# Kernel optimization log

Measured on AMD Instinct MI355X. Metric: run time of the kernel, lower is better.

The kernel has to match this reference:

```python
import jax, jax.numpy as jnp
import numpy as np

D_MODEL = 768
N_HEADS = 12
D_K = D_MODEL // N_HEADS
NEG = -1e9


def setup_inputs() -> dict:
    key = jax.random.key(0)
    ks = jax.random.split(key, 9)
    B, S = 4, 2048
    s = 1.0 / np.sqrt(D_MODEL)
    inp = {
        "x": jax.random.normal(ks[0], (B, S, D_MODEL), dtype=jnp.float32),
        "mask": jnp.tril(jnp.ones((S, S), dtype=jnp.int32))[None, None, :, :],
        "Wq": jax.random.normal(ks[1], (D_MODEL, D_MODEL), dtype=jnp.float32) * s,
        "bq": jnp.zeros((D_MODEL,), dtype=jnp.float32),
        "Wk": jax.random.normal(ks[2], (D_MODEL, D_MODEL), dtype=jnp.float32) * s,
        "bk": jnp.zeros((D_MODEL,), dtype=jnp.float32),
        "Wv": jax.random.normal(ks[3], (D_MODEL, D_MODEL), dtype=jnp.float32) * s,
        "bv": jnp.zeros((D_MODEL,), dtype=jnp.float32),
        "Wo": jax.random.normal(ks[4], (D_MODEL, D_MODEL), dtype=jnp.float32) * s,
        "bo": jnp.zeros((D_MODEL,), dtype=jnp.float32),
    }
    return inp


def reference(x, mask, Wq, bq, Wk, bk, Wv, bv, Wo, bo):
    B, S, _ = x.shape
    # projections; weights stored [in, out] so y = x @ W + b
    def proj(W, b):
        return (x @ W + b).reshape(B, S, N_HEADS, D_K).transpose(0, 2, 1, 3)  # [B,H,S,Dk]
    q = proj(Wq, bq)
    k = proj(Wk, bk)
    v = proj(Wv, bv)
    scores = jnp.einsum("bhsd,bhtd->bhst", q, k) / jnp.sqrt(jnp.float32(D_K))
    scores = jnp.where(mask == 0, jnp.float32(NEG), scores)
    probs = jax.nn.softmax(scores, axis=-1)  # dropout is identity in eval mode
    ctx = jnp.einsum("bhst,bhtd->bhsd", probs, v)
    ctx = ctx.transpose(0, 2, 1, 3).reshape(B, S, D_MODEL)
    return ctx @ Wo + bo
```

## Files before the change

### kernel.cpp

```cpp
#include <hip/hip_runtime.h>
#include <hip/hip_bf16.h>

#define D_MODEL 768
#define NH 12
#define DK 64
#define SL 2048
#define BB 4
#define QL2E 0.18033688011112042f

typedef __attribute__((ext_vector_type(8))) short bf16x8;
typedef __attribute__((ext_vector_type(4))) float f32x4;

__device__ __forceinline__ unsigned short f2bf(float f) {
    unsigned u = __float_as_uint(f);
    u += 0x7FFFu + ((u >> 16) & 1u);
    return (unsigned short)(u >> 16);
}
__device__ __forceinline__ unsigned pkbf(float a, float b) {
    __hip_bfloat162 h = __float22bfloat162_rn(make_float2(a, b));
    unsigned u; __builtin_memcpy(&u, &h, 4); return u;
}
__device__ __forceinline__ void gll16(const unsigned short* g, unsigned short* l) {
    __builtin_amdgcn_global_load_lds(
        (const __attribute__((address_space(1))) unsigned int*)g,
        (__attribute__((address_space(3))) unsigned int*)l, 16, 0, 0);
}

__global__ __launch_bounds__(256)
void prep_kernel(const float* __restrict__ x, unsigned short* __restrict__ xb,
                 const float* __restrict__ Wq, const float* __restrict__ Wk,
                 const float* __restrict__ Wv, const float* __restrict__ Wo,
                 unsigned short* __restrict__ Wqkv_t,
                 unsigned short* __restrict__ Wo_t)
{
    __shared__ float t[32][33];
    const int bid = blockIdx.x;
    const int tid = threadIdx.x;
    if (bid < 6144) {
        const size_t i = ((size_t)bid * 256 + tid) * 4;
        float4 v = *(const float4*)(x + i);
        *(uint2*)(xb + i) = make_uint2(pkbf(v.x, v.y), pkbf(v.z, v.w));
    } else {
        const int nb = bid - 6144;
        const int z  = nb / 576;
        const int rem = nb - z * 576;
        const int k0 = (rem / 24) * 32, n0 = (rem % 24) * 32;
        const float* W = (z == 0) ? Wq : (z == 1) ? Wk : (z == 2) ? Wv : Wo;
        unsigned short* Wt = (z < 3) ? (Wqkv_t + (size_t)z * 768 * 768) : Wo_t;
        const int tx = tid & 31, ty = tid >> 5;
        #pragma unroll
        for (int i = 0; i < 4; ++i)
            t[ty + 8 * i][tx] = W[(size_t)(k0 + ty + 8 * i) * 768 + n0 + tx];
        __syncthreads();
        #pragma unroll
        for (int i = 0; i < 4; ++i)
            Wt[(size_t)(n0 + ty + 8 * i) * 768 + k0 + tx] = f2bf(t[tx][ty + 8 * i]);
    }
}

#define GEMM_DECLS                                                             \
    const int tid  = threadIdx.x;                                              \
    const int wv   = tid >> 6;                                                 \
    const int lane = tid & 63;                                                 \
    const int l15  = lane & 15;                                                \
    const int quad = lane >> 4;                                                \
    const int wm = wv >> 1, wn = wv & 1;                                       \
    (void)wm; (void)wn;

#define GEMM_LOOP(Ap, Bp)                                                      \
    f32x4 acc[4][4];                                                           \
    _Pragma("unroll")                                                          \
    for (int i = 0; i < 4; ++i)                                                \
        _Pragma("unroll")                                                      \
        for (int j = 0; j < 4; ++j) acc[i][j] = (f32x4){0.f, 0.f, 0.f, 0.f};   \
    auto stageg = [&](int k0, int bi) {                                        \
        _Pragma("unroll")                                                      \
        for (int t = 0; t < 2; ++t) {                                          \
            const int cib = wv * 128 + t * 64;                                 \
            const int ci  = cib + lane;                                        \
            gll16(Ap + (size_t)(bm + (ci >> 2)) * 768 + k0 + (ci & 3) * 8,     \
                  &smem[bi][cib * 8]);                                         \
            gll16(Bp + (size_t)(bn + (ci >> 2)) * 768 + k0 + (ci & 3) * 8,     \
                  &smem[2 + bi][cib * 8]);                                     \
        }                                                                      \
    };                                                                         \
    stageg(0, 0);                                                              \
    for (int k0 = 0; k0 < 768; k0 += 32) {                                     \
        __syncthreads();                                                       \
        if (k0 + 32 < 768) stageg(k0 + 32, ((k0 >> 5) + 1) & 1);               \
        const int bi = (k0 >> 5) & 1;                                          \
        bf16x8 af[4], bfr[4];                                                  \
        _Pragma("unroll")                                                      \
        for (int mt = 0; mt < 4; ++mt)                                         \
            af[mt] = *(const bf16x8*)&smem[bi][(wm * 64 + mt * 16 + l15) * 32 + quad * 8]; \
        _Pragma("unroll")                                                      \
        for (int nt = 0; nt < 4; ++nt)                                         \
            bfr[nt] = *(const bf16x8*)&smem[2 + bi][(wn * 64 + nt * 16 + l15) * 32 + quad * 8]; \
        _Pragma("unroll")                                                      \
        for (int mt = 0; mt < 4; ++mt)                                         \
            _Pragma("unroll")                                                  \
            for (int nt = 0; nt < 4; ++nt)                                     \
                acc[mt][nt] = __builtin_amdgcn_mfma_f32_16x16x32_bf16(         \
                    af[mt], bfr[nt], acc[mt][nt], 0, 0, 0);                    \
    }

__global__ __launch_bounds__(256)
void gemm_qkv(const unsigned short* __restrict__ Wt,
              const unsigned short* __restrict__ X,
              const unsigned short* __restrict__ Wvt,
              const float* __restrict__ bq, const float* __restrict__ bk,
              const float* __restrict__ bv,
              unsigned short* __restrict__ Qo, unsigned short* __restrict__ Ko,
              unsigned short* __restrict__ Vo)
{
    __shared__ unsigned short smem[4][128 * 32];
    const int bid = blockIdx.x;
    GEMM_DECLS

    if (bid < 768) {
        const int bm = (bid / 64) * 128;
        const int bn = (bid % 64) * 128;
        GEMM_LOOP(Wt, X)

        const int proj = (bm >= 768);
        const float osc = proj ? 1.0f : QL2E;
        const float* bias = proj ? bk : bq;
        unsigned short* out = proj ? Ko : Qo;
        const int mb0 = bm - proj * 768;

        unsigned short* se = &smem[0][0];
        unsigned short* ew = se + wv * 4096;
        __syncthreads();
        #pragma unroll
        for (int nt = 0; nt < 4; ++nt) {
            const int row = nt * 16 + l15;
            #pragma unroll
            for (int mt = 0; mt < 4; ++mt) {
                const int ml = mb0 + wm * 64 + mt * 16 + quad * 4;
                const float4 bb = *(const float4*)&bias[ml];
                const float v0 = (acc[mt][nt][0] + bb.x) * osc;
                const float v1 = (acc[mt][nt][1] + bb.y) * osc;
                const float v2 = (acc[mt][nt][2] + bb.z) * osc;
                const float v3 = (acc[mt][nt][3] + bb.w) * osc;
                const int s   = mt * 4 + quad;
                const int ssw = s ^ ((l15 & 7) << 1);
                *(uint2*)(ew + row * 64 + ssw * 4) =
                    make_uint2(pkbf(v0, v1), pkbf(v2, v3));
            }
        }
        __syncthreads();
        const int h0 = mb0 >> 6;
        #pragma unroll
        for (int p = 0; p < 8; ++p) {
            const int g    = p * 256 + tid;
            const int c    = g & 7;
            const int s128 = (g >> 3) & 127;
            const int hh   = g >> 10;
            const int row  = s128 & 63;
            const bf16x8 val = *(const bf16x8*)(se + (hh * 2 + (s128 >> 6)) * 4096 +
                                row * 64 + ((c ^ (row & 7)) * 8));
            const int sg = bn + s128;
            const int b = sg >> 11, ss = sg & (SL - 1);
            *(bf16x8*)(out + (((size_t)(b * NH + h0 + hh) * SL + ss) * DK) + c * 8) = val;
        }
    } else {
        const int vid = bid - 768;
        const int bm = (vid / 6) * 128;
        const int bn = (vid % 6) * 128;
        GEMM_LOOP(X, Wvt)

        const int b = bm >> 11, sbase = bm & (SL - 1);
        unsigned short* se = &smem[0][0];
        unsigned short* ew = se + wv * 4096;
        const int sw = l15 & 7;
        __syncthreads();
        #pragma unroll
        for (int nt = 0; nt < 4; ++nt) {
            const int coll = bn + wn * 64 + nt * 16 + l15;
            const float bb = bv[coll];
            const int row = nt * 16 + l15;
            #pragma unroll
            for (int mt = 0; mt < 4; ++mt) {
                const float v0 = acc[mt][nt][0] + bb;
                const float v1 = acc[mt][nt][1] + bb;
                const float v2 = acc[mt][nt][2] + bb;
                const float v3 = acc[mt][nt][3] + bb;
                const int s   = mt * 4 + quad;
                const int ssw = s ^ (sw << 1);
                *(uint2*)(ew + row * 64 + ssw * 4) =
                    make_uint2(pkbf(v0, v1), pkbf(v2, v3));
            }
        }
        __syncthreads();
        const int h0 = bn >> 6;
        #pragma unroll
        for (int p = 0; p < 8; ++p) {
            const int r = (p & 3) * 32 + (tid >> 3);
            const int c = (tid & 7) + (p >> 2) * 8;
            const int wv2 = ((c >> 3) << 1) | (r >> 6);
            const bf16x8 val = *(const bf16x8*)(se + wv2 * 4096 +
                                (r & 63) * 64 + (((c & 7) ^ (r & 7)) * 8));
            const int h = h0 + (r >> 6), dk = r & 63;
            *(bf16x8*)(Vo + ((size_t)(b * NH + h) * DK + dk) * SL +
                       sbase + c * 8) = val;
        }
    }
}

__global__ __launch_bounds__(256)
void gemm_o(const unsigned short* __restrict__ X,
            const unsigned short* __restrict__ Wot,
            const float* __restrict__ bo,
            float* __restrict__ out)
{
    __shared__ unsigned short sA[2][64 * 32];
    __shared__ unsigned short sB[2][128 * 32];
    const int tid  = threadIdx.x;
    const int wv   = tid >> 6;
    const int lane = tid & 63;
    const int l15  = lane & 15;
    const int quad = lane >> 4;
    const int wm = wv >> 1, wn = wv & 1;
    const int bm = (blockIdx.x & 127) * 64;
    const int bn = (blockIdx.x >> 7) * 128;

    f32x4 acc[2][4];
    #pragma unroll
    for (int i = 0; i < 2; ++i)
        #pragma unroll
        for (int j = 0; j < 4; ++j) acc[i][j] = (f32x4){0.f, 0.f, 0.f, 0.f};

    auto stageg = [&](int k0, int bi) {
        #pragma unroll
        for (int t = 0; t < 3; ++t) {
            const int cib = wv * 192 + t * 64;
            const int ci  = cib + lane;
            if (cib < 256) {
                gll16(X + (size_t)(bm + (ci >> 2)) * 768 + k0 + (ci & 3) * 8,
                      &sA[bi][cib * 8]);
            } else {
                const int cb = ci - 256;
                gll16(Wot + (size_t)(bn + (cb >> 2)) * 768 + k0 + (cb & 3) * 8,
                      &sB[bi][(cib - 256) * 8]);
            }
        }
    };

    stageg(0, 0);
    for (int k0 = 0; k0 < 768; k0 += 32) {
        __syncthreads();
        if (k0 + 32 < 768) stageg(k0 + 32, ((k0 >> 5) + 1) & 1);
        const int bi = (k0 >> 5) & 1;
        bf16x8 af[2], bfr[4];
        #pragma unroll
        for (int mt = 0; mt < 2; ++mt)
            af[mt] = *(const bf16x8*)&sA[bi][(wm * 32 + mt * 16 + l15) * 32 + quad * 8];
        #pragma unroll
        for (int nt = 0; nt < 4; ++nt)
            bfr[nt] = *(const bf16x8*)&sB[bi][(wn * 64 + nt * 16 + l15) * 32 + quad * 8];
        #pragma unroll
        for (int mt = 0; mt < 2; ++mt)
            #pragma unroll
            for (int nt = 0; nt < 4; ++nt)
                acc[mt][nt] = __builtin_amdgcn_mfma_f32_16x16x32_bf16(
                    af[mt], bfr[nt], acc[mt][nt], 0, 0, 0);
    }

    #pragma unroll
    for (int nt = 0; nt < 4; ++nt) {
        const int col = bn + wn * 64 + nt * 16 + l15;
        const float bb = bo[col];
        #pragma unroll
        for (int mt = 0; mt < 2; ++mt)
            #pragma unroll
            for (int reg = 0; reg < 4; ++reg) {
                const int row = bm + wm * 32 + mt * 16 + quad * 4 + reg;
                out[(size_t)row * 768 + col] = acc[mt][nt][reg] + bb;
            }
    }
}

__global__ __launch_bounds__(256)
void attn_kernel(const unsigned short* __restrict__ Q,
                 const unsigned short* __restrict__ K,
                 const unsigned short* __restrict__ Vt,
                 unsigned short* __restrict__ ctx)
{
    __shared__ unsigned short sK[2][64 * 64];
    __shared__ unsigned short sV[2][64 * 64];
    __shared__ unsigned short sPt[4][16 * 64];

    const int tid  = threadIdx.x;
    const int w    = tid >> 6;
    const int lane = tid & 63;
    const int l15  = lane & 15;
    const int quad = lane >> 4;
    const int sw   = l15 & 7;
    const int g    = blockIdx.x;
    const int grp  = g >> 3;
    const int pr   = grp & 15;
    const int bh   = (g & 7) * 6 + (grp >> 4);
    const int qlo = pr, qhi = 31 - pr;
    const int b = bh / NH, h = bh - b * NH;

    const unsigned short* Qb = Q  + (size_t)bh * SL * DK;
    const unsigned short* Kb = K  + (size_t)bh * SL * DK;
    const unsigned short* Vb = Vt + (size_t)bh * DK * SL;
    unsigned short* pw = &sPt[w][l15 * 64];

    bf16x8 bql0, bql1, bqh0, bqh1;
    {
        const unsigned short* ql = Qb + (size_t)(qlo * 64 + w * 16 + l15) * DK + quad * 8;
        const unsigned short* qh = Qb + (size_t)(qhi * 64 + w * 16 + l15) * DK + quad * 8;
        bql0 = *(const bf16x8*)ql;  bql1 = *(const bf16x8*)(ql + 32);
        bqh0 = *(const bf16x8*)qh;  bqh1 = *(const bf16x8*)(qh + 32);
    }

    f32x4 o_lo[4], o_hi[4];
    #pragma unroll
    for (int nt = 0; nt < 4; ++nt) {
        o_lo[nt] = (f32x4){0.f, 0.f, 0.f, 0.f};
        o_hi[nt] = (f32x4){0.f, 0.f, 0.f, 0.f};
    }
    float lsum_lo = 0.f, lsum_hi = 0.f;

    auto stage = [&](int kt, int bi) {
        #pragma unroll
        for (int t = 0; t < 2; ++t) {
            const int cib = w * 128 + t * 64;
            const int ci  = cib + lane;
            const int r   = ci >> 3;
            const int cs  = (ci & 7) ^ (r & 7);
            gll16(Kb + (size_t)(kt * 64 + r) * DK + cs * 8, &sK[bi][cib * 8]);
            gll16(Vb + (size_t)r * SL + kt * 64 + cs * 8,   &sV[bi][cib * 8]);
        }
    };

    auto tile = [&](const bf16x8& bq0, const bf16x8& bq1,
                    f32x4* o, float& lsum, bool diag, int bi) {
        f32x4 st[4];
        #pragma unroll
        for (int mt = 0; mt < 4; ++mt) {
            const unsigned short* kr = &sK[bi][(mt * 16 + l15) * 64];
            bf16x8 ak0 = *(const bf16x8*)(kr + ((quad ^ sw) * 8));
            bf16x8 ak1 = *(const bf16x8*)(kr + (((quad + 4) ^ sw) * 8));
            f32x4 c = (f32x4){0.f, 0.f, 0.f, 0.f};
            c = __builtin_amdgcn_mfma_f32_16x16x32_bf16(ak0, bq0, c, 0, 0, 0);
            st[mt] = __builtin_amdgcn_mfma_f32_16x16x32_bf16(ak1, bq1, c, 0, 0, 0);
        }
        const int qrow = w * 16 + l15;
        #pragma unroll
        for (int mt = 0; mt < 4; ++mt) {
            float p[4];
            #pragma unroll
            for (int reg = 0; reg < 4; ++reg) {
                const int kl = mt * 16 + quad * 4 + reg;
                float v = __builtin_amdgcn_exp2f(st[mt][reg]);
                if (diag && kl > qrow) v = 0.f;
                p[reg] = v;
                lsum += v;
            }
            const int s   = mt * 4 + quad;
            const int ssw = s ^ (sw << 1);
            *(uint2*)(pw + ssw * 4) =
                make_uint2(pkbf(p[0], p[1]), pkbf(p[2], p[3]));
        }
        bf16x8 ap0 = *(const bf16x8*)(pw + ((quad ^ sw) * 8));
        bf16x8 ap1 = *(const bf16x8*)(pw + (((quad + 4) ^ sw) * 8));
        #pragma unroll
        for (int nt = 0; nt < 4; ++nt) {
            const unsigned short* vr = &sV[bi][(nt * 16 + l15) * 64];
            bf16x8 v0 = *(const bf16x8*)(vr + ((quad ^ sw) * 8));
            bf16x8 v1 = *(const bf16x8*)(vr + (((quad + 4) ^ sw) * 8));
            o[nt] = __builtin_amdgcn_mfma_f32_16x16x32_bf16(ap0, v0, o[nt], 0, 0, 0);
            o[nt] = __builtin_amdgcn_mfma_f32_16x16x32_bf16(ap1, v1, o[nt], 0, 0, 0);
        }
    };

    stage(0, 0);
    for (int kt = 0; kt <= qhi; ++kt) {
        __syncthreads();
        if (kt < qhi) stage(kt + 1, (kt + 1) & 1);
        const int bi = kt & 1;
        tile(bqh0, bqh1, o_hi, lsum_hi, kt == qhi, bi);
        if (kt <= qlo) tile(bql0, bql1, o_lo, lsum_lo, kt == qlo, bi);
    }

    lsum_lo += __shfl_xor(lsum_lo, 16);
    lsum_lo += __shfl_xor(lsum_lo, 32);
    lsum_hi += __shfl_xor(lsum_hi, 16);
    lsum_hi += __shfl_xor(lsum_hi, 32);
    const float inv_lo = 1.f / lsum_lo;
    const float inv_hi = 1.f / lsum_hi;
    float il[4], ih[4];
    #pragma unroll
    for (int reg = 0; reg < 4; ++reg) {
        il[reg] = __shfl(inv_lo, quad * 4 + reg);
        ih[reg] = __shfl(inv_hi, quad * 4 + reg);
    }

    #pragma unroll
    for (int nt = 0; nt < 4; ++nt)
        #pragma unroll
        for (int reg = 0; reg < 4; ++reg) {
            const int qlr = qlo * 64 + w * 16 + quad * 4 + reg;
            const int qhr = qhi * 64 + w * 16 + quad * 4 + reg;
            const int cc = h * DK + nt * 16 + l15;
            ctx[((size_t)(b * SL + qlr)) * D_MODEL + cc] = f2bf(o_lo[nt][reg] * il[reg]);
            ctx[((size_t)(b * SL + qhr)) * D_MODEL + cc] = f2bf(o_hi[nt][reg] * ih[reg]);
        }
}

extern "C" void kernel_launch(void* const* d_in, const int* in_sizes, int n_in,
                              void* d_out, int out_size, void* d_ws, size_t ws_size,
                              hipStream_t stream)
{
    const float* x  = (const float*)d_in[0];
    const float* Wq = (const float*)d_in[2];
    const float* bq = (const float*)d_in[3];
    const float* Wk = (const float*)d_in[4];
    const float* bk = (const float*)d_in[5];
    const float* Wv = (const float*)d_in[6];
    const float* bv = (const float*)d_in[7];
    const float* Wo = (const float*)d_in[8];
    const float* bo = (const float*)d_in[9];

    unsigned short* ws = (unsigned short*)d_ws;
    const size_t per = (size_t)BB * NH * SL * DK;
    unsigned short* Qb   = ws;
    unsigned short* Kb   = ws + per;
    unsigned short* Vtb  = ws + 2 * per;
    unsigned short* XbCb = ws + 3 * per;

    unsigned short* Wqkv_m = (unsigned short*)d_in[1];
    unsigned short* Wv_m   = Wqkv_m + (size_t)2 * 768 * 768;
    unsigned short* Wo_m   = Wqkv_m + (size_t)3 * 768 * 768;

    dim3 blk(256);
    prep_kernel<<<8448, blk, 0, stream>>>(x, XbCb, Wq, Wk, Wv, Wo, Wqkv_m, Wo_m);
    gemm_qkv<<<1152, blk, 0, stream>>>(Wqkv_m, XbCb, Wv_m, bq, bk, bv, Qb, Kb, Vtb);
    attn_kernel<<<768, blk, 0, stream>>>(Qb, Kb, Vtb, XbCb);
    gemm_o<<<768, blk, 0, stream>>>(XbCb, Wo_m, bo, (float*)d_out);
}
```

Baseline: 227.9 us.

## Load K/V fragments directly from global into registers, drop LDS staging

The attention kernel stops staging K and V tiles into double-buffered shared memory with async global-to-LDS loads and block barriers. Each wave now loads its K and V MFMA fragments straight from global memory into registers every iteration, so the __syncthreads calls go away. The P scratch buffers are split per lo/hi tile, and launch bounds request 3 blocks per SM. The trade is that each of the 4 waves reloads the same K/V data, which costs redundant global/L2 traffic and exposes load latency with no prefetch, in exchange for no barriers and less LDS use.

Result: slower. 334.4 us (+46.8%).

```diff
diff --git a/kernel.cpp b/kernel.cpp
--- a/kernel.cpp
+++ b/kernel.cpp
@@ -280,15 +280,13 @@
     }
 }
 
-__global__ __launch_bounds__(256)
+__global__ __launch_bounds__(256, 3)
 void attn_kernel(const unsigned short* __restrict__ Q,
                  const unsigned short* __restrict__ K,
                  const unsigned short* __restrict__ Vt,
                  unsigned short* __restrict__ ctx)
 {
-    __shared__ unsigned short sK[2][64 * 64];
-    __shared__ unsigned short sV[2][64 * 64];
-    __shared__ unsigned short sPt[4][16 * 64];
+    __shared__ unsigned short sPt[8][16 * 64];
 
     const int tid  = threadIdx.x;
     const int w    = tid >> 6;
@@ -306,7 +304,8 @@
     const unsigned short* Qb = Q  + (size_t)bh * SL * DK;
     const unsigned short* Kb = K  + (size_t)bh * SL * DK;
     const unsigned short* Vb = Vt + (size_t)bh * DK * SL;
-    unsigned short* pw = &sPt[w][l15 * 64];
+    unsigned short* pwh = &sPt[w][l15 * 64];
+    unsigned short* pwl = &sPt[4 + w][l15 * 64];
 
     bf16x8 bql0, bql1, bqh0, bqh1;
     {
@@ -324,29 +323,16 @@
     }
     float lsum_lo = 0.f, lsum_hi = 0.f;
 
-    auto stage = [&](int kt, int bi) {
-        #pragma unroll
-        for (int t = 0; t < 2; ++t) {
-            const int cib = w * 128 + t * 64;
-            const int ci  = cib + lane;
-            const int r   = ci >> 3;
-            const int cs  = (ci & 7) ^ (r & 7);
-            gll16(Kb + (size_t)(kt * 64 + r) * DK + cs * 8, &sK[bi][cib * 8]);
-            gll16(Vb + (size_t)r * SL + kt * 64 + cs * 8,   &sV[bi][cib * 8]);
-        }
-    };
-
     auto tile = [&](const bf16x8& bq0, const bf16x8& bq1,
-                    f32x4* o, float& lsum, bool diag, int bi) {
+                    f32x4* o, float& lsum, bool diag, unsigned short* pw,
+                    const bf16x8* kf0, const bf16x8* kf1,
+                    const bf16x8* vf0, const bf16x8* vf1) {
         f32x4 st[4];
         #pragma unroll
         for (int mt = 0; mt < 4; ++mt) {
-            const unsigned short* kr = &sK[bi][(mt * 16 + l15) * 64];
-            bf16x8 ak0 = *(const bf16x8*)(kr + ((quad ^ sw) * 8));
-            bf16x8 ak1 = *(const bf16x8*)(kr + (((quad + 4) ^ sw) * 8));
             f32x4 c = (f32x4){0.f, 0.f, 0.f, 0.f};
-            c = __builtin_amdgcn_mfma_f32_16x16x32_bf16(ak0, bq0, c, 0, 0, 0);
-            st[mt] = __builtin_amdgcn_mfma_f32_16x16x32_bf16(ak1, bq1, c, 0, 0, 0);
+            c = __builtin_amdgcn_mfma_f32_16x16x32_bf16(kf0[mt], bq0, c, 0, 0, 0);
+            st[mt] = __builtin_amdgcn_mfma_f32_16x16x32_bf16(kf1[mt], bq1, c, 0, 0, 0);
         }
         const int qrow = w * 16 + l15;
         #pragma unroll
@@ -369,21 +355,30 @@
         bf16x8 ap1 = *(const bf16x8*)(pw + (((quad + 4) ^ sw) * 8));
         #pragma unroll
         for (int nt = 0; nt < 4; ++nt) {
-            const unsigned short* vr = &sV[bi][(nt * 16 + l15) * 64];
-            bf16x8 v0 = *(const bf16x8*)(vr + ((quad ^ sw) * 8));
-            bf16x8 v1 = *(const bf16x8*)(vr + (((quad + 4) ^ sw) * 8));
-            o[nt] = __builtin_amdgcn_mfma_f32_16x16x32_bf16(ap0, v0, o[nt], 0, 0, 0);
-            o[nt] = __builtin_amdgcn_mfma_f32_16x16x32_bf16(ap1, v1, o[nt], 0, 0, 0);
+            o[nt] = __builtin_amdgcn_mfma_f32_16x16x32_bf16(ap0, vf0[nt], o[nt], 0, 0, 0);
+            o[nt] = __builtin_amdgcn_mfma_f32_16x16x32_bf16(ap1, vf1[nt], o[nt], 0, 0, 0);
         }
     };
 
-    stage(0, 0);
     for (int kt = 0; kt <= qhi; ++kt) {
-        __syncthreads();
-        if (kt < qhi) stage(kt + 1, (kt + 1) & 1);
-        const int bi = kt & 1;
-        tile(bqh0, bqh1, o_hi, lsum_hi, kt == qhi, bi);
-        if (kt <= qlo) tile(bql0, bql1, o_lo, lsum_lo, kt == qlo, bi);
+        bf16x8 kf0[4], kf1[4], vf0[4], vf1[4];
+        #pragma unroll
+        for (int mt = 0; mt < 4; ++mt) {
+            const unsigned short* kr =
+                Kb + (size_t)(kt * 64 + mt * 16 + l15) * DK + quad * 8;
+            kf0[mt] = *(const bf16x8*)kr;
+            kf1[mt] = *(const bf16x8*)(kr + 32);
+        }
+        #pragma unroll
+        for (int nt = 0; nt < 4; ++nt) {
+            const unsigned short* vr =
+                Vb + (size_t)(nt * 16 + l15) * SL + kt * 64 + quad * 8;
+            vf0[nt] = *(const bf16x8*)vr;
+            vf1[nt] = *(const bf16x8*)(vr + 32);
+        }
+        tile(bqh0, bqh1, o_hi, lsum_hi, kt == qhi, pwh, kf0, kf1, vf0, vf1);
+        if (kt <= qlo)
+            tile(bql0, bql1, o_lo, lsum_lo, kt == qlo, pwl, kf0, kf1, vf0, vf1);
     }
 
     lsum_lo += __shfl_xor(lsum_lo, 16);
```

## Split paired causal query tiles into separate blocks ordered longest-first

Applied to the files above, without the earlier changes.

The attention kernel stops pairing a low and a high query tile per block. It now launches one block per query tile, doubling the grid, and orders blocks so the longest causal rows are scheduled first. It also adds a min-blocks-per-CU hint of 4 to bound register use. This gives finer load balancing and more occupancy in exchange for losing the shared K/V tile reuse between the two paired query tiles, which raises K/V traffic.

Measured after the change: 210.5 us. 1.08x faster.

```diff
diff --git a/kernel.cpp b/kernel.cpp
--- a/kernel.cpp
+++ b/kernel.cpp
@@ -280,7 +280,7 @@
     }
 }
 
-__global__ __launch_bounds__(256)
+__global__ __launch_bounds__(256, 4)
 void attn_kernel(const unsigned short* __restrict__ Q,
                  const unsigned short* __restrict__ K,
                  const unsigned short* __restrict__ Vt,
@@ -297,10 +297,10 @@
     const int quad = lane >> 4;
     const int sw   = l15 & 7;
     const int g    = blockIdx.x;
-    const int grp  = g >> 3;
-    const int pr   = grp & 15;
-    const int bh   = (g & 7) * 6 + (grp >> 4);
-    const int qlo = pr, qhi = 31 - pr;
+    const int xcd  = g & 7;
+    const int rem  = g >> 3;
+    const int bh   = xcd * 6 + (rem % 6);
+    const int qt   = 31 - (rem / 6);
     const int b = bh / NH, h = bh - b * NH;
 
     const unsigned short* Qb = Q  + (size_t)bh * SL * DK;
@@ -308,21 +308,16 @@
     const unsigned short* Vb = Vt + (size_t)bh * DK * SL;
     unsigned short* pw = &sPt[w][l15 * 64];
 
-    bf16x8 bql0, bql1, bqh0, bqh1;
+    bf16x8 bq0, bq1;
     {
-        const unsigned short* ql = Qb + (size_t)(qlo * 64 + w * 16 + l15) * DK + quad * 8;
-        const unsigned short* qh = Qb + (size_t)(qhi * 64 + w * 16 + l15) * DK + quad * 8;
-        bql0 = *(const bf16x8*)ql;  bql1 = *(const bf16x8*)(ql + 32);
-        bqh0 = *(const bf16x8*)qh;  bqh1 = *(const bf16x8*)(qh + 32);
-    }
-
-    f32x4 o_lo[4], o_hi[4];
+        const unsigned short* ql = Qb + (size_t)(qt * 64 + w * 16 + l15) * DK + quad * 8;
+        bq0 = *(const bf16x8*)ql;  bq1 = *(const bf16x8*)(ql + 32);
+    }
+
+    f32x4 o[4];
     #pragma unroll
-    for (int nt = 0; nt < 4; ++nt) {
-        o_lo[nt] = (f32x4){0.f, 0.f, 0.f, 0.f};
-        o_hi[nt] = (f32x4){0.f, 0.f, 0.f, 0.f};
-    }
-    float lsum_lo = 0.f, lsum_hi = 0.f;
+    for (int nt = 0; nt < 4; ++nt) o[nt] = (f32x4){0.f, 0.f, 0.f, 0.f};
+    float lsum = 0.f;
 
     auto stage = [&](int kt, int bi) {
         #pragma unroll
@@ -336,8 +331,7 @@
         }
     };
 
-    auto tile = [&](const bf16x8& bq0, const bf16x8& bq1,
-                    f32x4* o, float& lsum, bool diag, int bi) {
+    auto tile = [&](bool diag, int bi) {
         f32x4 st[4];
         #pragma unroll
         for (int mt = 0; mt < 4; ++mt) {
@@ -378,36 +372,27 @@
     };
 
     stage(0, 0);
-    for (int kt = 0; kt <= qhi; ++kt) {
-        __syncthreads();
-        if (kt < qhi) stage(kt + 1, (kt + 1) & 1);
-        const int bi = kt & 1;
-        tile(bqh0, bqh1, o_hi, lsum_hi, kt == qhi, bi);
-        if (kt <= qlo) tile(bql0, bql1, o_lo, lsum_lo, kt == qlo, bi);
-    }
-
-    lsum_lo += __shfl_xor(lsum_lo, 16);
-    lsum_lo += __shfl_xor(lsum_lo, 32);
-    lsum_hi += __shfl_xor(lsum_hi, 16);
-    lsum_hi += __shfl_xor(lsum_hi, 32);
-    const float inv_lo = 1.f / lsum_lo;
-    const float inv_hi = 1.f / lsum_hi;
-    float il[4], ih[4];
+    for (int kt = 0; kt <= qt; ++kt) {
+        __syncthreads();
+        if (kt < qt) stage(kt + 1, (kt + 1) & 1);
+        tile(kt == qt, kt & 1);
+    }
+
+    lsum += __shfl_xor(lsum, 16);
+    lsum += __shfl_xor(lsum, 32);
+    const float inv = 1.f / lsum;
+    float il[4];
     #pragma unroll
-    for (int reg = 0; reg < 4; ++reg) {
-        il[reg] = __shfl(inv_lo, quad * 4 + reg);
-        ih[reg] = __shfl(inv_hi, quad * 4 + reg);
-    }
+    for (int reg = 0; reg < 4; ++reg)
+        il[reg] = __shfl(inv, quad * 4 + reg);
 
     #pragma unroll
     for (int nt = 0; nt < 4; ++nt)
         #pragma unroll
         for (int reg = 0; reg < 4; ++reg) {
-            const int qlr = qlo * 64 + w * 16 + quad * 4 + reg;
-            const int qhr = qhi * 64 + w * 16 + quad * 4 + reg;
+            const int qr = qt * 64 + w * 16 + quad * 4 + reg;
             const int cc = h * DK + nt * 16 + l15;
-            ctx[((size_t)(b * SL + qlr)) * D_MODEL + cc] = f2bf(o_lo[nt][reg] * il[reg]);
-            ctx[((size_t)(b * SL + qhr)) * D_MODEL + cc] = f2bf(o_hi[nt][reg] * ih[reg]);
+            ctx[((size_t)(b * SL + qr)) * D_MODEL + cc] = f2bf(o[nt][reg] * il[reg]);
         }
 }
 
@@ -439,6 +424,6 @@
     dim3 blk(256);
     prep_kernel<<<8448, blk, 0, stream>>>(x, XbCb, Wq, Wk, Wv, Wo, Wqkv_m, Wo_m);
     gemm_qkv<<<1152, blk, 0, stream>>>(Wqkv_m, XbCb, Wv_m, bq, bk, bv, Qb, Kb, Vtb);
-    attn_kernel<<<768, blk, 0, stream>>>(Qb, Kb, Vtb, XbCb);
+    attn_kernel<<<1536, blk, 0, stream>>>(Qb, Kb, Vtb, XbCb);
     gemm_o<<<768, blk, 0, stream>>>(XbCb, Wo_m, bo, (float*)d_out);
 }
```
